# Performance work log

Hardware: AMD Instinct MI355X
Metric: run time of the kernel (lower is better)

The kernel has to match this reference:

```python
import jax, jax.numpy as jnp
import numpy as np

# Model dims (LLaMA-2-70B-style GQA layer)
B, S, E = 2, 2048, 4096
HQ, HKV, D = 32, 8, 128          # q heads, kv heads, head_dim = E // HQ
KV_REP = HQ // HKV               # 4
SCALE = 1.0 / np.sqrt(E)         # NOTE: module uses 1/sqrt(embed_dim), not 1/sqrt(head_dim)


def setup_inputs() -> dict:
    key = jax.random.key(0)
    ks = jax.random.split(key, 6)
    x = jax.random.normal(ks[0], (B, S, E), dtype=jnp.float32)
    input_pos = jnp.arange(S, dtype=jnp.int32)
    # rotary frequencies: cos/sin pairs, shape [S, D//2, 2]
    inv_freq = 1.0 / (10000.0 ** (jnp.arange(0, D, 2, dtype=jnp.float32) / D))
    t = jnp.arange(S, dtype=jnp.float32)
    ang = jnp.outer(t, inv_freq)                      # [S, D//2]
    freqs_cis = jnp.stack([jnp.cos(ang), jnp.sin(ang)], axis=-1)
    std = E ** -0.5
    wq = jax.random.normal(ks[1], (E, HQ * D), dtype=jnp.float32) * std
    wk = jax.random.normal(ks[2], (E, HKV * D), dtype=jnp.float32) * std
    wv = jax.random.normal(ks[3], (E, HKV * D), dtype=jnp.float32) * std
    wo = jax.random.normal(ks[4], (HQ * D, E), dtype=jnp.float32) * std
    k_cache = jnp.zeros((B, HKV, S, D), dtype=jnp.float32)
    v_cache = jnp.zeros((B, HKV, S, D), dtype=jnp.float32)
    return {"x": x, "input_pos": input_pos, "freqs_cis": freqs_cis,
            "wq": wq, "wk": wk, "wv": wv, "wo": wo,
            "k_cache": k_cache, "v_cache": v_cache}


def _apply_rope(t, cos, sin):
    # t: [B, S, H, D]; cos/sin: [1, S, 1, D//2]
    tp = t.reshape(*t.shape[:-1], D // 2, 2)
    tr, ti = tp[..., 0], tp[..., 1]
    out = jnp.stack([tr * cos - ti * sin, tr * sin + ti * cos], axis=-1)
    return out.reshape(t.shape)


def reference(x, input_pos, freqs_cis, wq, wk, wv, wo, k_cache, v_cache):
    bsz, seq, _ = x.shape
    q = (x @ wq).reshape(bsz, seq, HQ, D)
    k = (x @ wk).reshape(bsz, seq, HKV, D)
    v = (x @ wv).reshape(bsz, seq, HKV, D)
    cos = freqs_cis[None, :, None, :, 0]
    sin = freqs_cis[None, :, None, :, 1]
    q = _apply_rope(q, cos, sin)
    k = _apply_rope(k, cos, sin)
    # [B, H, S, D]
    q = q.transpose(0, 2, 1, 3)
    k = k.transpose(0, 2, 1, 3)
    v = v.transpose(0, 2, 1, 3)
    # KV-cache scatter update at input_pos
    k = k_cache.at[:, :, input_pos].set(k)
    v = v_cache.at[:, :, input_pos].set(v)
    # GQA repeat_interleave along head dim
    k = jnp.repeat(k, KV_REP, axis=1)
    v = jnp.repeat(v, KV_REP, axis=1)
    scores = jnp.einsum('bhqd,bhkd->bhqk', q, k) * SCALE
    causal = jnp.tril(jnp.ones((seq, k.shape[2]), dtype=bool))
    scores = jnp.where(causal[None, None], scores, jnp.finfo(scores.dtype).min)
    attn = jax.nn.softmax(scores, axis=-1)
    out = jnp.einsum('bhqk,bhkd->bhqd', attn, v)
    out = out.transpose(0, 2, 1, 3).reshape(bsz, seq, E)
    return out @ wo
```

## Files before the change

kernel.cpp:

```cpp
#include <hip/hip_runtime.h>


typedef __bf16 bf16;
typedef __attribute__((ext_vector_type(8))) __bf16 bf16x8;
typedef __attribute__((ext_vector_type(4))) float f32x4;

#define NEG_INF (-__builtin_inff())
#define SCLOG2E 0.02254248593737584f

__device__ __forceinline__ f32x4 mfma16(bf16x8 a, bf16x8 b, f32x4 c) {
  return __builtin_amdgcn_mfma_f32_16x16x32_bf16(a, b, c, 0, 0, 0);
}

__device__ __forceinline__ void gload_lds16(const void* g, void* l) {
  __builtin_amdgcn_global_load_lds(
      (const __attribute__((address_space(1))) unsigned int*)g,
      (__attribute__((address_space(3))) unsigned int*)l, 16, 0, 0);
}

__global__ __launch_bounds__(256) void convert_x(const float* __restrict__ x,
                                                 bf16* __restrict__ xP) {
  int p = blockIdx.x * 256 + threadIdx.x;
  int blk = p >> 10;
  int q = p & 1023;
  int k2 = q >> 7, row = q & 127;
  int mb = blk >> 6, kb = blk & 63;
  size_t m = (size_t)mb * 128 + row;
  size_t k = (size_t)kb * 64 + k2 * 8;
  const float* src = x + m * 4096 + k;
  float4 a = *(const float4*)(src);
  float4 b = *(const float4*)(src + 4);
  bf16x8 o;
  o[0] = (bf16)a.x; o[1] = (bf16)a.y; o[2] = (bf16)a.z; o[3] = (bf16)a.w;
  o[4] = (bf16)b.x; o[5] = (bf16)b.y; o[6] = (bf16)b.z; o[7] = (bf16)b.w;
  *(bf16x8*)(xP + (size_t)p * 8) = o;
}

__global__ __launch_bounds__(256) void tpack(const float* __restrict__ W,
                                             int Nw, int n_base,
                                             bf16* __restrict__ P) {
  __shared__ __align__(16) float tile[64][65];
  int t = threadIdx.x;
  int n0 = blockIdx.x * 64;
  int k0 = blockIdx.y * 64;
#pragma unroll
  for (int i = 0; i < 16; ++i) {
    int u = t + 256 * i;
    int kr = u >> 6, nc = u & 63;
    tile[kr][nc] = W[(size_t)(k0 + kr) * Nw + n0 + nc];
  }
  __syncthreads();
  int kb = blockIdx.y;
#pragma unroll
  for (int i = 0; i < 2; ++i) {
    int c = t + 256 * i;
    int k2 = c >> 6, nl = c & 63;
    int n = n_base + n0 + nl;
    bf16x8 o;
#pragma unroll
    for (int j = 0; j < 8; ++j) o[j] = (bf16)tile[k2 * 8 + j][nl];
    size_t flat = ((size_t)(n >> 7) * 64 + kb) * 8192 + k2 * 1024 + (n & 127) * 8;
    *(bf16x8*)(P + flat) = o;
  }
}

template <int STORE_BF16>
__global__ __launch_bounds__(256) void gemm_packed(const bf16* __restrict__ Ap,
                                                   const bf16* __restrict__ Bp,
                                                   void* __restrict__ Cv,
                                                   int KB, int ldC) {
  __shared__ __align__(16) bf16 lds[16384];
  const int t = threadIdx.x;
  const int w = t >> 6, lane = t & 63, q = lane >> 4, l15 = lane & 15;
  const int wm = w >> 1, wn = w & 1;
  const int mb = blockIdx.y, nb = blockIdx.x;

  f32x4 acc[4][4];
#pragma unroll
  for (int i = 0; i < 4; ++i)
#pragma unroll
    for (int j = 0; j < 4; ++j) acc[i][j] = (f32x4){0.f, 0.f, 0.f, 0.f};

  const bf16* Ab = Ap + (size_t)mb * KB * 8192;
  const bf16* Bb = Bp + (size_t)nb * KB * 8192;

  for (int kb = 0; kb < KB; ++kb) {
    __syncthreads();
    const bf16* ga = Ab + (size_t)kb * 8192;
    const bf16* gb = Bb + (size_t)kb * 8192;
#pragma unroll
    for (int i = 0; i < 4; ++i) {
      int c = w * 256 + i * 64;
      gload_lds16(ga + (size_t)(c + lane) * 8, (void*)&lds[c * 8]);
      gload_lds16(gb + (size_t)(c + lane) * 8, (void*)&lds[8192 + c * 8]);
    }
    __syncthreads();
#pragma unroll
    for (int s = 0; s < 2; ++s) {
      bf16x8 af[4], bfr[4];
#pragma unroll
      for (int i = 0; i < 4; ++i) {
        af[i] = *(const bf16x8*)&lds[(((s * 4 + q) << 7) + wm * 64 + i * 16 + l15) * 8];
        bfr[i] = *(const bf16x8*)&lds[8192 + (((s * 4 + q) << 7) + wn * 64 + i * 16 + l15) * 8];
      }
#pragma unroll
      for (int i = 0; i < 4; ++i)
#pragma unroll
        for (int j = 0; j < 4; ++j) acc[i][j] = mfma16(af[i], bfr[j], acc[i][j]);
    }
  }

  const int r0 = mb * 128 + wm * 64, c0 = nb * 128 + wn * 64;
  if (STORE_BF16) {
    bf16* C = (bf16*)Cv;
#pragma unroll
    for (int i = 0; i < 4; ++i)
#pragma unroll
      for (int j = 0; j < 4; ++j)
#pragma unroll
        for (int r = 0; r < 4; ++r)
          C[(size_t)(r0 + i * 16 + q * 4 + r) * ldC + c0 + j * 16 + l15] =
              (bf16)acc[i][j][r];
  } else {
    float* C = (float*)Cv;
#pragma unroll
    for (int i = 0; i < 4; ++i)
#pragma unroll
      for (int j = 0; j < 4; ++j)
#pragma unroll
        for (int r = 0; r < 4; ++r)
          C[(size_t)(r0 + i * 16 + q * 4 + r) * ldC + c0 + j * 16 + l15] =
              acc[i][j][r];
  }
}

__global__ __launch_bounds__(256) void kvpack(const bf16* __restrict__ qkv,
                                              const float* __restrict__ fr,
                                              bf16* __restrict__ Kp,
                                              bf16* __restrict__ Vp) {
  __shared__ __align__(16) bf16 vt[64 * 136];
  const int t = threadIdx.x;
  const int sblk = blockIdx.x;
  const int bkvh = blockIdx.y;
  const int b = bkvh >> 3, kvh = bkvh & 7;
  const size_t tbase = ((size_t)bkvh * 32 + sblk) * 8192;
  const size_t row0 = (size_t)b * 2048 + sblk * 64;

#pragma unroll
  for (int it = 0; it < 4; ++it) {
    int c = it * 256 + t;
    int s_l = c >> 4, dc = c & 15;
    int s = sblk * 64 + s_l;
    bf16x8 v = *(const bf16x8*)(qkv + (row0 + s_l) * 6144 + 4096 + kvh * 128 + dc * 8);
    const float* frow = fr + (size_t)s * 128 + dc * 8;
    bf16x8 o;
#pragma unroll
    for (int p = 0; p < 4; ++p) {
      float2 cs = *(const float2*)(frow + p * 2);
      float tr = (float)v[2 * p], ti = (float)v[2 * p + 1];
      o[2 * p] = (bf16)(tr * cs.x - ti * cs.y);
      o[2 * p + 1] = (bf16)(tr * cs.y + ti * cs.x);
    }
    *(bf16x8*)(Kp + tbase + dc * 512 + s_l * 8) = o;
  }

#pragma unroll
  for (int it = 0; it < 4; ++it) {
    int c = it * 256 + t;
    int s_l = c >> 4, dc = c & 15;
    bf16x8 v = *(const bf16x8*)(qkv + (row0 + s_l) * 6144 + 5120 + kvh * 128 + dc * 8);
    *(bf16x8*)&vt[s_l * 136 + dc * 8] = v;
  }
  __syncthreads();
#pragma unroll
  for (int it = 0; it < 4; ++it) {
    int c = it * 256 + t;
    int s8 = c >> 7, d = c & 127;
    bf16x8 o;
#pragma unroll
    for (int j = 0; j < 8; ++j) o[j] = vt[(s8 * 8 + j) * 136 + d];
    *(bf16x8*)(Vp + tbase + (size_t)c * 8) = o;
  }
}

__global__ __launch_bounds__(256, 2) void attn_kernel(
    const bf16* __restrict__ qkv, const bf16* __restrict__ Kp,
    const bf16* __restrict__ Vp, const float* __restrict__ fr,
    bf16* __restrict__ Op) {
  __shared__ __align__(16) bf16 ktile[2][8192];
  __shared__ __align__(16) bf16 vtile[2][8192];
  __shared__ __align__(16) bf16 pb[4][1024];

  const int t = threadIdx.x;
  const int w = t >> 6, lane = t & 63, q = lane >> 4, l15 = lane & 15;
  const int bh = blockIdx.y, b = bh >> 5, h = bh & 31, kvh = h >> 2;
  const int y = blockIdx.x;
  const int q0s[2] = {y * 64 + w * 16, (31 - y) * 64 + w * 16};
  const int nt = 32 - y;

  bf16x8 qf[2][4];
#pragma unroll
  for (int g = 0; g < 2; ++g) {
    int row = q0s[g] + l15;
    const bf16* qrow = qkv + ((size_t)(b * 2048 + row)) * 6144 + h * 128;
    const float* frow = fr + (size_t)row * 128;
#pragma unroll
    for (int tk = 0; tk < 4; ++tk) {
      bf16x8 v = *(const bf16x8*)(qrow + tk * 32 + q * 8);
      bf16x8 o;
#pragma unroll
      for (int p = 0; p < 4; ++p) {
        float2 cs = *(const float2*)(frow + (tk * 16 + q * 4 + p) * 2);
        float tr = (float)v[2 * p], ti = (float)v[2 * p + 1];
        o[2 * p] = (bf16)(tr * cs.x - ti * cs.y);
        o[2 * p + 1] = (bf16)(tr * cs.y + ti * cs.x);
      }
      qf[g][tk] = o;
    }
  }

  f32x4 O[2][8];
#pragma unroll
  for (int g = 0; g < 2; ++g)
#pragma unroll
    for (int j = 0; j < 8; ++j) O[g][j] = (f32x4){0.f, 0.f, 0.f, 0.f};
  float mrow[2][4], lrow[2][4];
#pragma unroll
  for (int g = 0; g < 2; ++g)
#pragma unroll
    for (int r = 0; r < 4; ++r) { mrow[g][r] = NEG_INF; lrow[g][r] = 0.f; }

  const bf16* Kbase = Kp + (size_t)(b * 8 + kvh) * 32 * 8192;
  const bf16* Vbase = Vp + (size_t)(b * 8 + kvh) * 32 * 8192;

#pragma unroll
  for (int i2 = 0; i2 < 4; ++i2) {
    int c = w * 256 + i2 * 64;
    gload_lds16(Kbase + (size_t)(c + lane) * 8, (void*)&ktile[0][c * 8]);
    gload_lds16(Vbase + (size_t)(c + lane) * 8, (void*)&vtile[0][c * 8]);
  }

  int cur = 0;
  for (int ti = 0; ti < nt; ++ti) {
    __syncthreads();

    if (ti + 1 < nt) {
      const bf16* Kt = Kbase + (size_t)(ti + 1) * 8192;
      const bf16* Vt = Vbase + (size_t)(ti + 1) * 8192;
#pragma unroll
      for (int i2 = 0; i2 < 4; ++i2) {
        int c = w * 256 + i2 * 64;
        gload_lds16(Kt + (size_t)(c + lane) * 8, (void*)&ktile[cur ^ 1][c * 8]);
        gload_lds16(Vt + (size_t)(c + lane) * 8, (void*)&vtile[cur ^ 1][c * 8]);
      }
    }

    const int kb = ti * 64;
    const bf16* kt = ktile[cur];
    const bf16* vt = vtile[cur];

#pragma unroll
    for (int g = 0; g < 2; ++g) {
      const int q0 = q0s[g];
      if (kb <= q0 + 15) {
        f32x4 sc[4];
#pragma unroll
        for (int jn = 0; jn < 4; ++jn) sc[jn] = (f32x4){0.f, 0.f, 0.f, 0.f};
        __builtin_amdgcn_s_setprio(1);
#pragma unroll
        for (int tk = 0; tk < 4; ++tk)
#pragma unroll
          for (int jn = 0; jn < 4; ++jn) {
            bf16x8 kf = *(const bf16x8*)&kt[(tk * 4 + q) * 512 + (jn * 16 + l15) * 8];
            sc[jn] = mfma16(qf[g][tk], kf, sc[jn]);
          }
        __builtin_amdgcn_s_setprio(0);

        const bool domask = (kb + 63 > q0);
        float alpha[4];
#pragma unroll
        for (int r = 0; r < 4; ++r) {
          int rowq = q0 + q * 4 + r;
          float vs[4];
          float vmax = NEG_INF;
#pragma unroll
          for (int jn = 0; jn < 4; ++jn) {
            float v = sc[jn][r] * SCLOG2E;
            if (domask && (kb + jn * 16 + l15 > rowq)) v = NEG_INF;
            vs[jn] = v;
            vmax = fmaxf(vmax, v);
          }
          vmax = fmaxf(vmax, __shfl_xor(vmax, 1));
          vmax = fmaxf(vmax, __shfl_xor(vmax, 2));
          vmax = fmaxf(vmax, __shfl_xor(vmax, 4));
          vmax = fmaxf(vmax, __shfl_xor(vmax, 8));
          float mn = fmaxf(mrow[g][r], vmax);
          float ms = fmaxf(mn, -1e30f);
          float al = exp2f(mrow[g][r] - ms);
          float sum = 0.f;
#pragma unroll
          for (int jn = 0; jn < 4; ++jn) {
            float p = exp2f(vs[jn] - ms);
            sum += p;
            pb[w][(2 * jn + (l15 >> 3)) * 128 + (q * 4 + r) * 8 + (l15 & 7)] =
                (bf16)p;
          }
          sum += __shfl_xor(sum, 1);
          sum += __shfl_xor(sum, 2);
          sum += __shfl_xor(sum, 4);
          sum += __shfl_xor(sum, 8);
          lrow[g][r] = lrow[g][r] * al + sum;
          mrow[g][r] = mn;
          alpha[r] = al;
        }

#pragma unroll
        for (int jn = 0; jn < 8; ++jn)
#pragma unroll
          for (int r = 0; r < 4; ++r) O[g][jn][r] *= alpha[r];
        __builtin_amdgcn_s_setprio(1);
#pragma unroll
        for (int kh = 0; kh < 2; ++kh) {
          bf16x8 a0 = *(const bf16x8*)&pb[w][(kh * 4 + q) * 128 + l15 * 8];
#pragma unroll
          for (int jn = 0; jn < 8; ++jn) {
            bf16x8 vf = *(const bf16x8*)&vt[(kh * 4 + q) * 1024 + (jn * 16 + l15) * 8];
            O[g][jn] = mfma16(a0, vf, O[g][jn]);
          }
        }
        __builtin_amdgcn_s_setprio(0);
      }
    }
    cur ^= 1;
  }

#pragma unroll
  for (int g = 0; g < 2; ++g)
#pragma unroll
    for (int r = 0; r < 4; ++r) {
      float inv = 1.0f / lrow[g][r];
      int m = b * 2048 + q0s[g] + q * 4 + r;
#pragma unroll
      for (int jn = 0; jn < 8; ++jn) {
        int col = h * 128 + jn * 16 + l15;
        size_t flat = ((size_t)(m >> 7) * 64 + (col >> 6)) * 8192 +
                      ((col >> 3) & 7) * 1024 + (m & 127) * 8 + (col & 7);
        Op[flat] = (bf16)(O[g][jn][r] * inv);
      }
    }
}

extern "C" void kernel_launch(void* const* d_in, const int* in_sizes, int n_in,
                              void* d_out, int out_size, void* d_ws,
                              size_t ws_size, hipStream_t stream) {
  const float* x = (const float*)d_in[0];
  const float* fr = (const float*)d_in[2];
  const float* wq = (const float*)d_in[3];
  const float* wk = (const float*)d_in[4];
  const float* wv = (const float*)d_in[5];
  const float* wo = (const float*)d_in[6];
  float* out = (float*)d_out;
  char* ws = (char*)d_ws;

  bf16* xP = (bf16*)(ws);
  bf16* WqkvP = (bf16*)(ws + 33554432ull);
  bf16* WoP = (bf16*)(ws + 83886080ull);
  bf16* qkv = (bf16*)(ws + 117440512ull);
  bf16* Kp = (bf16*)(ws + 33554432ull);
  bf16* Vp = (bf16*)(ws + 41943040ull);
  bf16* attnP = xP;

  convert_x<<<dim3(8192), dim3(256), 0, stream>>>(x, xP);
  tpack<<<dim3(64, 64), dim3(256), 0, stream>>>(wq, 4096, 0, WqkvP);
  tpack<<<dim3(16, 64), dim3(256), 0, stream>>>(wk, 1024, 4096, WqkvP);
  tpack<<<dim3(16, 64), dim3(256), 0, stream>>>(wv, 1024, 5120, WqkvP);
  tpack<<<dim3(64, 64), dim3(256), 0, stream>>>(wo, 4096, 0, WoP);
  gemm_packed<1><<<dim3(48, 32), dim3(256), 0, stream>>>(xP, WqkvP, qkv, 64, 6144);
  kvpack<<<dim3(32, 16), dim3(256), 0, stream>>>(qkv, fr, Kp, Vp);
  attn_kernel<<<dim3(16, 64), dim3(256), 0, stream>>>(qkv, Kp, Vp, fr, attnP);
  gemm_packed<0><<<dim3(32, 32), dim3(256), 0, stream>>>(attnP, WoP, out, 64, 4096);
}
```

Baseline: 829.5 us.

## Rewrite packed GEMM as 256x256 double-buffered 8-wave pipelined kernel

The packed bf16 GEMM used for the QKV and output projections now computes 256x256 tiles with 512 threads (8 waves, each holding 128x64 of accumulators). The K-loop double-buffers global-to-LDS loads, prefetching tile kt+2 while tile kt is computed. MFMA work is split into four phases separated by explicit barriers and s_setprio, so compute interleaves with LDS reads and prefetch. This targets the global load latency and low data reuse of the old single-buffered 128x128 kernel. In exchange it uses 128KB of LDS and many more registers, and launches fewer blocks (384 and 256).

```diff
diff --git a/kernel.cpp b/kernel.cpp
--- a/kernel.cpp
+++ b/kernel.cpp
@@ -7,6 +7,19 @@
 
 #define NEG_INF (-__builtin_inff())
 #define SCLOG2E 0.02254248593737584f
+
+#define SCHED0() __builtin_amdgcn_sched_barrier(0)
+#define BAR()                         \
+  do {                                \
+    SCHED0();                         \
+    __builtin_amdgcn_s_barrier();     \
+    SCHED0();                         \
+  } while (0)
+#define LGKM0()                                        \
+  do {                                                 \
+    asm volatile("s_waitcnt lgkmcnt(0)" ::: "memory"); \
+    SCHED0();                                          \
+  } while (0)
 
 __device__ __forceinline__ f32x4 mfma16(bf16x8 a, bf16x8 b, f32x4 c) {
   return __builtin_amdgcn_mfma_f32_16x16x32_bf16(a, b, c, 0, 0, 0);
@@ -65,72 +78,162 @@
 }
 
 template <int STORE_BF16>
-__global__ __launch_bounds__(256) void gemm_packed(const bf16* __restrict__ Ap,
-                                                   const bf16* __restrict__ Bp,
-                                                   void* __restrict__ Cv,
-                                                   int KB, int ldC) {
-  __shared__ __align__(16) bf16 lds[16384];
+__global__ __launch_bounds__(512, 2) void gemm_packed(const bf16* __restrict__ Ap,
+                                                      const bf16* __restrict__ Bp,
+                                                      void* __restrict__ Cv,
+                                                      int KB, int ldC) {
+  __shared__ __align__(16) bf16 sA[2][16384];
+  __shared__ __align__(16) bf16 sB[2][16384];
   const int t = threadIdx.x;
-  const int w = t >> 6, lane = t & 63, q = lane >> 4, l15 = lane & 15;
-  const int wm = w >> 1, wn = w & 1;
-  const int mb = blockIdx.y, nb = blockIdx.x;
-
-  f32x4 acc[4][4];
-#pragma unroll
-  for (int i = 0; i < 4; ++i)
-#pragma unroll
-    for (int j = 0; j < 4; ++j) acc[i][j] = (f32x4){0.f, 0.f, 0.f, 0.f};
-
-  const bf16* Ab = Ap + (size_t)mb * KB * 8192;
-  const bf16* Bb = Bp + (size_t)nb * KB * 8192;
-
-  for (int kb = 0; kb < KB; ++kb) {
-    __syncthreads();
-    const bf16* ga = Ab + (size_t)kb * 8192;
-    const bf16* gb = Bb + (size_t)kb * 8192;
-#pragma unroll
-    for (int i = 0; i < 4; ++i) {
-      int c = w * 256 + i * 64;
-      gload_lds16(ga + (size_t)(c + lane) * 8, (void*)&lds[c * 8]);
-      gload_lds16(gb + (size_t)(c + lane) * 8, (void*)&lds[8192 + c * 8]);
-    }
-    __syncthreads();
-#pragma unroll
-    for (int s = 0; s < 2; ++s) {
-      bf16x8 af[4], bfr[4];
-#pragma unroll
-      for (int i = 0; i < 4; ++i) {
-        af[i] = *(const bf16x8*)&lds[(((s * 4 + q) << 7) + wm * 64 + i * 16 + l15) * 8];
-        bfr[i] = *(const bf16x8*)&lds[8192 + (((s * 4 + q) << 7) + wn * 64 + i * 16 + l15) * 8];
+  const int wid = t >> 6, lane = t & 63, q = lane >> 4, l15 = lane & 15;
+  const int wm = wid >> 2, wn = wid & 3;
+  const int MB = blockIdx.y, NB = blockIdx.x;
+  const int rb = (wn & 1) * 64;
+
+  f32x4 acc[8][4];
+#pragma unroll
+  for (int m = 0; m < 8; ++m)
+#pragma unroll
+    for (int n = 0; n < 4; ++n) acc[m][n] = (f32x4){0.f, 0.f, 0.f, 0.f};
+
+  const bf16* A0 = Ap + (size_t)(MB * 2 + 0) * KB * 8192;
+  const bf16* A1 = Ap + (size_t)(MB * 2 + 1) * KB * 8192;
+  const bf16* B0 = Bp + (size_t)(NB * 2 + 0) * KB * 8192;
+  const bf16* B1 = Bp + (size_t)(NB * 2 + 1) * KB * 8192;
+
+#define STAGE_TILE(kt2, buf)                                                   \
+  do {                                                                         \
+    const bf16* gA0 = A0 + (size_t)(kt2)*8192;                                 \
+    const bf16* gA1 = A1 + (size_t)(kt2)*8192;                                 \
+    const bf16* gB0 = B0 + (size_t)(kt2)*8192;                                 \
+    const bf16* gB1 = B1 + (size_t)(kt2)*8192;                                 \
+    _Pragma("unroll") for (int g = 0; g < 2; ++g) {                            \
+      int c = (wid * 2 + g) * 64;                                              \
+      gload_lds16(gA0 + (size_t)(c + lane) * 8, (void*)&sA[buf][c * 8]);       \
+      gload_lds16(gA1 + (size_t)(c + lane) * 8, (void*)&sA[buf][8192 + c * 8]);\
+      gload_lds16(gB0 + (size_t)(c + lane) * 8, (void*)&sB[buf][c * 8]);       \
+      gload_lds16(gB1 + (size_t)(c + lane) * 8, (void*)&sB[buf][8192 + c * 8]);\
+    }                                                                          \
+  } while (0)
+
+  STAGE_TILE(0, 0);
+  STAGE_TILE(1, 1);
+  asm volatile("s_waitcnt vmcnt(8)" ::: "memory");
+  BAR();
+
+  for (int kt = 0; kt < KB; ++kt) {
+    const int cur = kt & 1;
+    const bf16* sAc = &sA[cur][wm * 8192];
+    const bf16* sBc = &sB[cur][(wn >> 1) * 8192];
+
+    bf16x8 aF[4][2], a2F[4][2], bF[4][2];
+
+#pragma unroll
+    for (int m = 0; m < 4; ++m)
+#pragma unroll
+      for (int ks = 0; ks < 2; ++ks)
+        aF[m][ks] = *(const bf16x8*)&sAc[(ks * 4 + q) * 1024 + (m * 16 + l15) * 8];
+#pragma unroll
+    for (int n = 0; n < 2; ++n)
+#pragma unroll
+      for (int ks = 0; ks < 2; ++ks)
+        bF[n][ks] = *(const bf16x8*)&sBc[(ks * 4 + q) * 1024 + (rb + n * 16 + l15) * 8];
+    BAR();
+    LGKM0();
+    __builtin_amdgcn_s_setprio(1);
+#pragma unroll
+    for (int m = 0; m < 4; ++m)
+#pragma unroll
+      for (int n = 0; n < 2; ++n)
+#pragma unroll
+        for (int ks = 0; ks < 2; ++ks)
+          acc[m][n] = mfma16(aF[m][ks], bF[n][ks], acc[m][n]);
+    __builtin_amdgcn_s_setprio(0);
+    BAR();
+
+#pragma unroll
+    for (int n = 2; n < 4; ++n)
+#pragma unroll
+      for (int ks = 0; ks < 2; ++ks)
+        bF[n][ks] = *(const bf16x8*)&sBc[(ks * 4 + q) * 1024 + (rb + n * 16 + l15) * 8];
+    BAR();
+    LGKM0();
+    __builtin_amdgcn_s_setprio(1);
+#pragma unroll
+    for (int m = 0; m < 4; ++m)
+#pragma unroll
+      for (int n = 2; n < 4; ++n)
+#pragma unroll
+        for (int ks = 0; ks < 2; ++ks)
+          acc[m][n] = mfma16(aF[m][ks], bF[n][ks], acc[m][n]);
+    __builtin_amdgcn_s_setprio(0);
+    BAR();
+
+#pragma unroll
+    for (int m = 0; m < 4; ++m)
+#pragma unroll
+      for (int ks = 0; ks < 2; ++ks)
+        a2F[m][ks] =
+            *(const bf16x8*)&sAc[(ks * 4 + q) * 1024 + ((m + 4) * 16 + l15) * 8];
+    BAR();
+    LGKM0();
+    __builtin_amdgcn_s_setprio(1);
+#pragma unroll
+    for (int m = 0; m < 4; ++m)
+#pragma unroll
+      for (int n = 0; n < 2; ++n)
+#pragma unroll
+        for (int ks = 0; ks < 2; ++ks)
+          acc[m + 4][n] = mfma16(a2F[m][ks], bF[n][ks], acc[m + 4][n]);
+    __builtin_amdgcn_s_setprio(0);
+    BAR();
+
+    const bool more = (kt + 2 < KB);
+    if (more) STAGE_TILE(kt + 2, cur);
+    BAR();
+    __builtin_amdgcn_s_setprio(1);
+#pragma unroll
+    for (int m = 0; m < 4; ++m)
+#pragma unroll
+      for (int n = 2; n < 4; ++n)
+#pragma unroll
+        for (int ks = 0; ks < 2; ++ks)
+          acc[m + 4][n] = mfma16(a2F[m][ks], bF[n][ks], acc[m + 4][n]);
+    __builtin_amdgcn_s_setprio(0);
+    BAR();
+
+    if (kt + 1 < KB) {
+      if (more) {
+        asm volatile("s_waitcnt vmcnt(8)" ::: "memory");
+      } else {
+        asm volatile("s_waitcnt vmcnt(0)" ::: "memory");
       }
-#pragma unroll
-      for (int i = 0; i < 4; ++i)
-#pragma unroll
-        for (int j = 0; j < 4; ++j) acc[i][j] = mfma16(af[i], bfr[j], acc[i][j]);
-    }
-  }
-
-  const int r0 = mb * 128 + wm * 64, c0 = nb * 128 + wn * 64;
+      BAR();
+    }
+  }
+#undef STAGE_TILE
+
+  const int r0 = MB * 256 + wm * 128, c0 = NB * 256 + wn * 64;
   if (STORE_BF16) {
     bf16* C = (bf16*)Cv;
 #pragma unroll
-    for (int i = 0; i < 4; ++i)
-#pragma unroll
-      for (int j = 0; j < 4; ++j)
+    for (int m = 0; m < 8; ++m)
+#pragma unroll
+      for (int n = 0; n < 4; ++n)
 #pragma unroll
         for (int r = 0; r < 4; ++r)
-          C[(size_t)(r0 + i * 16 + q * 4 + r) * ldC + c0 + j * 16 + l15] =
-              (bf16)acc[i][j][r];
+          C[(size_t)(r0 + m * 16 + q * 4 + r) * ldC + c0 + n * 16 + l15] =
+              (bf16)acc[m][n][r];
   } else {
     float* C = (float*)Cv;
 #pragma unroll
-    for (int i = 0; i < 4; ++i)
-#pragma unroll
-      for (int j = 0; j < 4; ++j)
+    for (int m = 0; m < 8; ++m)
+#pragma unroll
+      for (int n = 0; n < 4; ++n)
 #pragma unroll
         for (int r = 0; r < 4; ++r)
-          C[(size_t)(r0 + i * 16 + q * 4 + r) * ldC + c0 + j * 16 + l15] =
-              acc[i][j][r];
+          C[(size_t)(r0 + m * 16 + q * 4 + r) * ldC + c0 + n * 16 + l15] =
+              acc[m][n][r];
   }
 }
 
@@ -375,8 +478,8 @@
   tpack<<<dim3(16, 64), dim3(256), 0, stream>>>(wk, 1024, 4096, WqkvP);
   tpack<<<dim3(16, 64), dim3(256), 0, stream>>>(wv, 1024, 5120, WqkvP);
   tpack<<<dim3(64, 64), dim3(256), 0, stream>>>(wo, 4096, 0, WoP);
-  gemm_packed<1><<<dim3(48, 32), dim3(256), 0, stream>>>(xP, WqkvP, qkv, 64, 6144);
+  gemm_packed<1><<<dim3(24, 16), dim3(512), 0, stream>>>(xP, WqkvP, qkv, 64, 6144);
   kvpack<<<dim3(32, 16), dim3(256), 0, stream>>>(qkv, fr, Kp, Vp);
   attn_kernel<<<dim3(16, 64), dim3(256), 0, stream>>>(qkv, Kp, Vp, fr, attnP);
-  gemm_packed<0><<<dim3(32, 32), dim3(256), 0, stream>>>(attnP, WoP, out, 64, 4096);
-}
+  gemm_packed<0><<<dim3(16, 16), dim3(512), 0, stream>>>(attnP, WoP, out, 64, 4096);
+}
```

New measurement: 901.5 us. 8.7% more time.

## Rewrite packed GEMM with 256x128 tiles, 512 threads and double-buffered async LDS loads

Applied to the files above, without the earlier changes.

The packed bf16 GEMM used for the QKV and output projections moves from a 128x128 tile with 4 waves and a single LDS buffer to a 256x128 tile with 8 waves. Global-to-LDS loads are double-buffered and split into half-k stages, using explicit vmcnt waits and barriers so the next tile loads while MFMAs run. It also raises wave priority around the MFMA block. The goal is to hide global load latency and cut LDS/global traffic per FLOP, at the cost of more LDS per block, fragile hand-tuned waitcnt accounting, and fewer blocks per grid.

```diff
diff --git a/kernel.cpp b/kernel.cpp
--- a/kernel.cpp
+++ b/kernel.cpp
@@ -65,72 +65,115 @@
 }
 
 template <int STORE_BF16>
-__global__ __launch_bounds__(256) void gemm_packed(const bf16* __restrict__ Ap,
+__global__ __launch_bounds__(512) void gemm_packed(const bf16* __restrict__ Ap,
                                                    const bf16* __restrict__ Bp,
                                                    void* __restrict__ Cv,
                                                    int KB, int ldC) {
-  __shared__ __align__(16) bf16 lds[16384];
+  __shared__ __align__(16) bf16 sA[2][16384];
+  __shared__ __align__(16) bf16 sB[2][8192];
   const int t = threadIdx.x;
-  const int w = t >> 6, lane = t & 63, q = lane >> 4, l15 = lane & 15;
-  const int wm = w >> 1, wn = w & 1;
-  const int mb = blockIdx.y, nb = blockIdx.x;
-
-  f32x4 acc[4][4];
-#pragma unroll
-  for (int i = 0; i < 4; ++i)
-#pragma unroll
-    for (int j = 0; j < 4; ++j) acc[i][j] = (f32x4){0.f, 0.f, 0.f, 0.f};
-
-  const bf16* Ab = Ap + (size_t)mb * KB * 8192;
-  const bf16* Bb = Bp + (size_t)nb * KB * 8192;
-
-  for (int kb = 0; kb < KB; ++kb) {
-    __syncthreads();
-    const bf16* ga = Ab + (size_t)kb * 8192;
-    const bf16* gb = Bb + (size_t)kb * 8192;
-#pragma unroll
-    for (int i = 0; i < 4; ++i) {
-      int c = w * 256 + i * 64;
-      gload_lds16(ga + (size_t)(c + lane) * 8, (void*)&lds[c * 8]);
-      gload_lds16(gb + (size_t)(c + lane) * 8, (void*)&lds[8192 + c * 8]);
-    }
-    __syncthreads();
-#pragma unroll
-    for (int s = 0; s < 2; ++s) {
-      bf16x8 af[4], bfr[4];
-#pragma unroll
-      for (int i = 0; i < 4; ++i) {
-        af[i] = *(const bf16x8*)&lds[(((s * 4 + q) << 7) + wm * 64 + i * 16 + l15) * 8];
-        bfr[i] = *(const bf16x8*)&lds[8192 + (((s * 4 + q) << 7) + wn * 64 + i * 16 + l15) * 8];
-      }
-#pragma unroll
-      for (int i = 0; i < 4; ++i)
-#pragma unroll
-        for (int j = 0; j < 4; ++j) acc[i][j] = mfma16(af[i], bfr[j], acc[i][j]);
-    }
-  }
-
-  const int r0 = mb * 128 + wm * 64, c0 = nb * 128 + wn * 64;
+  const int wid = t >> 6, lane = t & 63, q = lane >> 4, l15 = lane & 15;
+  const int wm = wid >> 2, wn = wid & 3;
+  const int MB = blockIdx.y, NB = blockIdx.x;
+
+  f32x4 acc[8][2];
+#pragma unroll
+  for (int m = 0; m < 8; ++m)
+#pragma unroll
+    for (int n = 0; n < 2; ++n) acc[m][n] = (f32x4){0.f, 0.f, 0.f, 0.f};
+
+  const bf16* A0 = Ap + (size_t)(MB * 2 + 0) * KB * 8192;
+  const bf16* A1 = Ap + (size_t)(MB * 2 + 1) * KB * 8192;
+  const bf16* B0 = Bp + (size_t)NB * KB * 8192;
+
+#define STAGE_REG(tc, buf, ks)                                  \
+  do {                                                          \
+    size_t go = (size_t)(tc)*8192 + (size_t)(ks)*4096 + t * 8;  \
+    int lo = (ks)*4096 + t * 8;                                 \
+    gload_lds16(A0 + go, (void*)&sA[buf][lo]);                  \
+    gload_lds16(A1 + go, (void*)&sA[buf][8192 + lo]);           \
+    gload_lds16(B0 + go, (void*)&sB[buf][lo]);                  \
+  } while (0)
+
+  STAGE_REG(0, 0, 0);
+  STAGE_REG(0, 0, 1);
+  STAGE_REG(1, 1, 0);
+  asm volatile("s_waitcnt vmcnt(6)" ::: "memory");
+  __builtin_amdgcn_s_barrier();
+
+  for (int kt = 0; kt < KB; ++kt) {
+    const int cur = kt & 1;
+    const bf16* sAc = &sA[cur][wm * 8192];
+    const bf16* sBc = &sB[cur][0];
+#pragma unroll
+    for (int ks = 0; ks < 2; ++ks) {
+      bf16x8 aF[8], bF[2];
+#pragma unroll
+      for (int m = 0; m < 8; ++m)
+        aF[m] = *(const bf16x8*)&sAc[(ks * 4 + q) * 1024 + (m * 16 + l15) * 8];
+#pragma unroll
+      for (int n = 0; n < 2; ++n)
+        bF[n] = *(const bf16x8*)&sBc[(ks * 4 + q) * 1024 +
+                                     (wn * 32 + n * 16 + l15) * 8];
+
+      if (ks == 0) {
+        if (kt + 1 < KB) STAGE_REG(kt + 1, cur ^ 1, 1);
+      } else {
+        if (kt + 2 < KB) STAGE_REG(kt + 2, cur, 0);
+      }
+
+      __builtin_amdgcn_s_barrier();
+      asm volatile("s_waitcnt lgkmcnt(0)" ::: "memory");
+      __builtin_amdgcn_sched_barrier(0);
+      __builtin_amdgcn_s_setprio(1);
+#pragma unroll
+      for (int m = 0; m < 8; ++m)
+#pragma unroll
+        for (int n = 0; n < 2; ++n) acc[m][n] = mfma16(aF[m], bF[n], acc[m][n]);
+      __builtin_amdgcn_s_setprio(0);
+
+      if (ks == 0) {
+        if (kt < KB - 1) {
+          asm volatile("s_waitcnt vmcnt(6)" ::: "memory");
+        } else {
+          asm volatile("s_waitcnt vmcnt(0)" ::: "memory");
+        }
+        __builtin_amdgcn_s_barrier();
+      } else {
+        if (kt < KB - 1) {
+          if (kt == KB - 2) {
+            asm volatile("s_waitcnt vmcnt(3)" ::: "memory");
+          } else {
+            asm volatile("s_waitcnt vmcnt(6)" ::: "memory");
+          }
+          __builtin_amdgcn_s_barrier();
+        }
+      }
+    }
+  }
+#undef STAGE_REG
+
+  const int r0 = MB * 256 + wm * 128, c0 = NB * 128 + wn * 32;
   if (STORE_BF16) {
     bf16* C = (bf16*)Cv;
 #pragma unroll
-    for (int i = 0; i < 4; ++i)
-#pragma unroll
-      for (int j = 0; j < 4; ++j)
+    for (int m = 0; m < 8; ++m)
+#pragma unroll
+      for (int n = 0; n < 2; ++n)
 #pragma unroll
         for (int r = 0; r < 4; ++r)
-          C[(size_t)(r0 + i * 16 + q * 4 + r) * ldC + c0 + j * 16 + l15] =
-              (bf16)acc[i][j][r];
+          C[(size_t)(r0 + m * 16 + q * 4 + r) * ldC + c0 + n * 16 + l15] =
+              (bf16)acc[m][n][r];
   } else {
     float* C = (float*)Cv;
 #pragma unroll
-    for (int i = 0; i < 4; ++i)
-#pragma unroll
-      for (int j = 0; j < 4; ++j)
+    for (int m = 0; m < 8; ++m)
+#pragma unroll
+      for (int n = 0; n < 2; ++n)
 #pragma unroll
         for (int r = 0; r < 4; ++r)
-          C[(size_t)(r0 + i * 16 + q * 4 + r) * ldC + c0 + j * 16 + l15] =
-              acc[i][j][r];
+          C[(size_t)(r0 + m * 16 + q * 4 + r) * ldC + c0 + n * 16 + l15] =
+              acc[m][n][r];
   }
 }
 
@@ -375,8 +418,8 @@
   tpack<<<dim3(16, 64), dim3(256), 0, stream>>>(wk, 1024, 4096, WqkvP);
   tpack<<<dim3(16, 64), dim3(256), 0, stream>>>(wv, 1024, 5120, WqkvP);
   tpack<<<dim3(64, 64), dim3(256), 0, stream>>>(wo, 4096, 0, WoP);
-  gemm_packed<1><<<dim3(48, 32), dim3(256), 0, stream>>>(xP, WqkvP, qkv, 64, 6144);
+  gemm_packed<1><<<dim3(48, 16), dim3(512), 0, stream>>>(xP, WqkvP, qkv, 64, 6144);
   kvpack<<<dim3(32, 16), dim3(256), 0, stream>>>(qkv, fr, Kp, Vp);
   attn_kernel<<<dim3(16, 64), dim3(256), 0, stream>>>(qkv, Kp, Vp, fr, attnP);
-  gemm_packed<0><<<dim3(32, 32), dim3(256), 0, stream>>>(attnP, WoP, out, 64, 4096);
-}
+  gemm_packed<0><<<dim3(32, 16), dim3(512), 0, stream>>>(attnP, WoP, out, 64, 4096);
+}
```

Result: slower. 853.8 us (+2.9%).
